# Kernel tuning notes

Measured on AMD Instinct MI355X. Metric: run time of the kernel, lower is better.

Reference implementation:

```python
import jax, jax.numpy as jnp
import numpy as np

N_NODES = 50000
N_EDGES = 800000
N_FEAT = 128
N_HID = 128
N_LAYER = 4
N_CLASS = 40


def setup_inputs() -> dict:
    key = jax.random.key(0)
    ks = jax.random.split(key, 8)
    x = jax.random.normal(ks[0], (N_NODES, N_FEAT), jnp.float32)
    edge_index = jax.random.randint(ks[1], (2, N_EDGES), 0, N_NODES, dtype=jnp.int64)
    s = 1.0 / np.float32(np.sqrt(N_HID))
    # n_feat == n_hid so all L conv weights stack into one [L, C, C] tensor
    convW = jax.random.normal(ks[2], (N_LAYER, N_HID, N_HID), jnp.float32) * s
    convb = jnp.zeros((N_LAYER, N_HID), jnp.float32)
    W_att = jax.random.normal(ks[3], (N_HID, N_HID), jnp.float32) * s
    a_att = jax.random.normal(ks[4], (N_HID,), jnp.float32) * s
    W_out = jax.random.normal(ks[5], (N_HID, N_CLASS), jnp.float32) * s
    b_out = jnp.zeros((N_CLASS,), jnp.float32)
    return dict(x=x, edge_index=edge_index, convW=convW, convb=convb,
                W_att=W_att, a_att=a_att, W_out=W_out, b_out=b_out)


def reference(x, edge_index, convW, convb, W_att, a_att, W_out, b_out):
    src, dst = edge_index[0], edge_index[1]
    N = x.shape[0]
    # GCN symmetric normalization with self-loops: deg = 1 + in-degree
    deg = jax.ops.segment_sum(jnp.ones_like(dst, dtype=jnp.float32), dst,
                              num_segments=N) + 1.0
    dinv = jax.lax.rsqrt(deg)
    enorm = (dinv[src] * dinv[dst])[:, None]   # per-edge norm
    snorm = (dinv * dinv)[:, None]             # self-loop norm

    hs = []
    h = x
    for l in range(N_LAYER):
        hW = h @ convW[l]                                          # [N, C]
        agg = jax.ops.segment_sum(hW[src] * enorm, dst, num_segments=N)
        agg = agg + hW * snorm                                     # self-loop
        h = jax.nn.relu(agg + convb[l])
        # dropout is identity at inference (training=False)
        hs.append(h)

    H = jnp.stack(hs, axis=1)                                      # [N, L, C]
    # additive attention over layers: alpha_l = softmax_l(a . tanh(W h_l))
    scores = jnp.tanh(H @ W_att) @ a_att                           # [N, L]
    alpha = jax.nn.softmax(scores, axis=1)
    fused = jnp.einsum('nl,nlc->nc', alpha, H)                     # [N, C]
    return fused @ W_out + b_out                                   # [N, n_class]
```

## Files before the change

### kernel.cpp

```cpp
#include <hip/hip_runtime.h>

#define NNODES 50000
#define NEDGES 800000
#define NCLASS 40
#define NBLK_SCAN 196
#define CNTB  3125
#define PREPB 320
#define WOUTB 24
#define GEMMB 782
#define XBLK  3125

typedef _Float16 half8  __attribute__((ext_vector_type(8)));
typedef float    floatx4 __attribute__((ext_vector_type(4)));

#define CSTR 136
#define SMEM_BYTES (64 * CSTR * 2 + 256)

__device__ __forceinline__ float fast_tanh(float x) {
    return 1.0f - 2.0f / (__expf(2.0f * x) + 1.0f);
}

__global__ __launch_bounds__(256) void k_pre(const int* __restrict__ dst, int* __restrict__ cnt,
                                             int* __restrict__ rank,
                                             const float* __restrict__ convW, const float* __restrict__ W_att,
                                             _Float16* __restrict__ WT,
                                             const float* __restrict__ Wout, _Float16* __restrict__ WoutT) {
    int bid = blockIdx.x, tid = threadIdx.x;
    if (bid < CNTB) {
        int e = bid * 256 + tid;
        rank[e] = atomicAdd(&cnt[dst[e]], 1);
    } else if (bid < CNTB + PREPB) {
        int idx = (bid - CNTB) * 256 + tid;
        int mat = idx >> 14, rem = idx & 16383;
        int j = rem & 7, lane = (rem >> 3) & 63, tile = rem >> 9;
        int l15 = lane & 15, quad = lane >> 4;
        int ct = tile & 7, kk = tile >> 3;
        int n = ct * 16 + l15, k = kk * 32 + quad * 8 + j;
        const float* src = (mat < 4) ? (convW + mat * 16384) : W_att;
        WT[idx] = (_Float16)src[k * 128 + n];
    } else {
        int idx = (bid - CNTB - PREPB) * 256 + tid;
        int j = idx & 7, lane = (idx >> 3) & 63, tile = idx >> 9;
        int l15 = lane & 15, quad = lane >> 4;
        int ct = tile % 3, kk = tile / 3;
        int n = ct * 16 + l15, k = kk * 32 + quad * 8 + j;
        WoutT[idx] = (n < NCLASS) ? (_Float16)Wout[k * NCLASS + n] : (_Float16)0.f;
    }
}

__global__ __launch_bounds__(256) void k_bsum(const int* __restrict__ cnt, int* __restrict__ bsum) {
    int t = threadIdx.x, b = blockIdx.x;
    int i = b * 256 + t;
    int c = (i < NNODES) ? cnt[i] : 0;
    int v = c;
    v += __shfl_xor(v, 1);  v += __shfl_xor(v, 2);  v += __shfl_xor(v, 4);
    v += __shfl_xor(v, 8);  v += __shfl_xor(v, 16); v += __shfl_xor(v, 32);
    __shared__ int ws[4];
    if ((t & 63) == 0) ws[t >> 6] = v;
    __syncthreads();
    if (t == 0) bsum[b] = ws[0] + ws[1] + ws[2] + ws[3];
}

__global__ __launch_bounds__(256) void k_offsets(const int* __restrict__ cnt, const int* __restrict__ bsum,
                                                 int* __restrict__ offsets, float* __restrict__ dinv) {
    int t = threadIdx.x, b = blockIdx.x;
    int i = b * 256 + t;
    int c = (i < NNODES) ? cnt[i] : 0;
    int pv = (t < b) ? bsum[t] : 0;
    int rv = pv;
    rv += __shfl_xor(rv, 1);  rv += __shfl_xor(rv, 2);  rv += __shfl_xor(rv, 4);
    rv += __shfl_xor(rv, 8);  rv += __shfl_xor(rv, 16); rv += __shfl_xor(rv, 32);
    __shared__ int wsum[4];
    __shared__ int part[256];
    if ((t & 63) == 0) wsum[t >> 6] = rv;
    part[t] = c;
    __syncthreads();
    int boff = wsum[0] + wsum[1] + wsum[2] + wsum[3];
#pragma unroll
    for (int d = 1; d < 256; d <<= 1) {
        int v = (t >= d) ? part[t - d] : 0;
        __syncthreads();
        part[t] += v;
        __syncthreads();
    }
    if (i < NNODES) {
        offsets[i] = boff + part[t] - c;
        dinv[i] = rsqrtf((float)c + 1.0f);
    }
    if (b == 0 && t == 0) offsets[NNODES] = NEDGES;
}

__device__ __forceinline__ void gemm_body_f32(const float* __restrict__ Av, const _Float16* __restrict__ WTf,
                                              const float* __restrict__ dinv, _Float16* __restrict__ C,
                                              int m0, char* smem) {
    _Float16 (*Csh)[CSTR] = (_Float16 (*)[CSTR])smem;
    float* sdinv = (float*)(smem + 64 * CSTR * 2);
    int tid = threadIdx.x;
    int wave = tid >> 6, lane = tid & 63;
    int quad = lane >> 4, l15 = lane & 15;
    int ko = quad * 8;

    if (tid < 64) {
        int r = m0 + tid; if (r > NNODES - 1) r = NNODES - 1;
        sdinv[tid] = dinv[r];
    }

    floatx4 acc[4][2];
#pragma unroll
    for (int rt = 0; rt < 4; ++rt)
#pragma unroll
        for (int ct = 0; ct < 2; ++ct) acc[rt][ct] = (floatx4){0.f, 0.f, 0.f, 0.f};

#pragma unroll
    for (int kk = 0; kk < 4; ++kk) {
        half8 a[4], b[2];
#pragma unroll
        for (int rt = 0; rt < 4; ++rt) {
            int row = m0 + rt * 16 + l15;
            if (row > NNODES - 1) row = NNODES - 1;
            const float* Ap = Av + (size_t)row * 128 + kk * 32 + ko;
            float4 f0 = *(const float4*)Ap;
            float4 f1 = *(const float4*)(Ap + 4);
            a[rt] = (half8){(_Float16)f0.x, (_Float16)f0.y, (_Float16)f0.z, (_Float16)f0.w,
                            (_Float16)f1.x, (_Float16)f1.y, (_Float16)f1.z, (_Float16)f1.w};
        }
#pragma unroll
        for (int ct = 0; ct < 2; ++ct)
            b[ct] = *(const half8*)&WTf[((kk * 8 + (wave * 2 + ct)) * 64 + lane) * 8];
#pragma unroll
        for (int rt = 0; rt < 4; ++rt)
#pragma unroll
            for (int ct = 0; ct < 2; ++ct)
                acc[rt][ct] = __builtin_amdgcn_mfma_f32_16x16x32_f16(a[rt], b[ct], acc[rt][ct], 0, 0, 0);
    }
    __syncthreads();

#pragma unroll
    for (int rt = 0; rt < 4; ++rt)
#pragma unroll
        for (int r = 0; r < 4; ++r) {
            float d = sdinv[rt * 16 + quad * 4 + r];
#pragma unroll
            for (int ct = 0; ct < 2; ++ct)
                Csh[rt * 16 + quad * 4 + r][wave * 32 + ct * 16 + l15] = (_Float16)(acc[rt][ct][r] * d);
        }
    __syncthreads();

    int row = tid >> 2, seg = tid & 3;
    int gm = m0 + row;
    if (gm < NNODES) {
#pragma unroll
        for (int j = 0; j < 4; ++j)
            *(half8*)(C + (size_t)gm * 128 + seg * 32 + j * 8) = *(const half8*)&Csh[row][seg * 32 + j * 8];
    }
}

__global__ __launch_bounds__(256) void k_fillgemm(const int* __restrict__ src, const int* __restrict__ dst,
                                                  const int* __restrict__ offsets, const int* __restrict__ rank,
                                                  int* __restrict__ esrc,
                                                  const float* __restrict__ x, const _Float16* __restrict__ WT,
                                                  const float* __restrict__ dinv, _Float16* __restrict__ C) {
    __shared__ __align__(16) char smem[SMEM_BYTES];
    int bid = blockIdx.x;
    if (bid < GEMMB) {
        gemm_body_f32(x, WT, dinv, C, bid * 64, smem);
    } else {
        int e = (bid - GEMMB) * 256 + threadIdx.x;
        int d = dst[e];
        esrc[offsets[d] + rank[e]] = src[e];
    }
}

template <bool HAS_GEMM>
__global__ __launch_bounds__(128) void k_layer(const _Float16* __restrict__ hin,
                                               const int* __restrict__ offsets, const int* __restrict__ esrc,
                                               const float* __restrict__ dinv, const float* __restrict__ bias,
                                               _Float16* __restrict__ hh,
                                               const _Float16* __restrict__ WTatt, const float* __restrict__ a_att,
                                               float* __restrict__ scores, int layer,
                                               const _Float16* __restrict__ WTnext, _Float16* __restrict__ hout) {
    __shared__ __align__(16) _Float16 h[16][CSTR];
    __shared__ float bsh[128];
    __shared__ float sdv[16];
    __shared__ float pp[2][16];
    int tid = threadIdx.x;
    bsh[tid] = bias[tid];
    int wave = tid >> 6, lane = tid & 63;
    int n0 = blockIdx.x * 16;

    {
        int nl = tid >> 3;
        int cl = tid & 7;
        int c16 = cl * 16;
        int n = n0 + nl;
        int beg = offsets[n], end = offsets[n + 1];
        float dn = dinv[n];
        const _Float16* sp = hin + (size_t)n * 128 + c16;
        half8 sv0 = *(const half8*)sp;
        half8 sv1 = *(const half8*)(sp + 8);

        float a[16];
#pragma unroll
        for (int u = 0; u < 16; ++u) a[u] = 0.f;

        int idxA[4]; float mskA[4];
#pragma unroll
        for (int i = 0; i < 4; ++i) {
            int ei = beg + i;
            int t = esrc[ei];
            bool ok = ei < end;
            idxA[i] = ok ? t : n;
            mskA[i] = ok ? 1.f : 0.f;
        }
        for (int e = beg; e < end; e += 4) {
            half8 v0[4], v1[4];
#pragma unroll
            for (int i = 0; i < 4; ++i) {
                const _Float16* p = hin + (size_t)idxA[i] * 128 + c16;
                v0[i] = *(const half8*)p;
                v1[i] = *(const half8*)(p + 8);
            }
            int idxB[4]; float mskB[4];
#pragma unroll
            for (int i = 0; i < 4; ++i) {
                int ei = e + 4 + i;
                int t = esrc[ei];
                bool ok = ei < end;
                idxB[i] = ok ? t : n;
                mskB[i] = ok ? 1.f : 0.f;
            }
#pragma unroll
            for (int i = 0; i < 4; ++i) {
                float m = mskA[i];
#pragma unroll
                for (int u = 0; u < 8; ++u) {
                    a[u]     += m * (float)v0[i][u];
                    a[8 + u] += m * (float)v1[i][u];
                }
            }
#pragma unroll
            for (int i = 0; i < 4; ++i) { idxA[i] = idxB[i]; mskA[i] = mskB[i]; }
        }
        __syncthreads();
        half8 o0, o1;
#pragma unroll
        for (int u = 0; u < 8; ++u) {
            float r0 = (a[u]     + (float)sv0[u]) * dn + bsh[c16 + u];
            float r1 = (a[8 + u] + (float)sv1[u]) * dn + bsh[c16 + 8 + u];
            o0[u] = (_Float16)fmaxf(r0, 0.f);
            o1[u] = (_Float16)fmaxf(r1, 0.f);
        }
        *(half8*)(hh + (size_t)n * 128 + c16)     = o0;
        *(half8*)(hh + (size_t)n * 128 + c16 + 8) = o1;
        *(half8*)&h[nl][c16]     = o0;
        *(half8*)&h[nl][c16 + 8] = o1;
        if (cl == 0) sdv[nl] = dn;
    }
    __syncthreads();

    int quad = lane >> 4, l15 = lane & 15;
    int ko = quad * 8;
    half8 af[4];
#pragma unroll
    for (int kk = 0; kk < 4; ++kk) af[kk] = *(const half8*)&h[l15][kk * 32 + ko];

    {
        float p[4] = {0.f, 0.f, 0.f, 0.f};
#pragma unroll
        for (int c2 = 0; c2 < 4; ++c2) {
            int ct = wave * 4 + c2;
            half8 b[4];
#pragma unroll
            for (int kk = 0; kk < 4; ++kk)
                b[kk] = *(const half8*)&WTatt[((kk * 8 + ct) * 64 + lane) * 8];
            floatx4 acc = (floatx4){0.f, 0.f, 0.f, 0.f};
#pragma unroll
            for (int kk = 0; kk < 4; ++kk)
                acc = __builtin_amdgcn_mfma_f32_16x16x32_f16(af[kk], b[kk], acc, 0, 0, 0);
            float av = a_att[ct * 16 + l15];
#pragma unroll
            for (int r = 0; r < 4; ++r) p[r] += av * fast_tanh(acc[r]);
        }
#pragma unroll
        for (int r = 0; r < 4; ++r) {
            float v = p[r];
            v += __shfl_xor(v, 1); v += __shfl_xor(v, 2);
            v += __shfl_xor(v, 4); v += __shfl_xor(v, 8);
            if (l15 == 0) pp[wave][quad * 4 + r] = v;
        }
    }
    __syncthreads();
    if (tid < 16) scores[(size_t)(n0 + tid) * 4 + layer] = pp[0][tid] + pp[1][tid];

    if (HAS_GEMM) {
        floatx4 acc[4];
#pragma unroll
        for (int c2 = 0; c2 < 4; ++c2) acc[c2] = (floatx4){0.f, 0.f, 0.f, 0.f};
#pragma unroll
        for (int c2 = 0; c2 < 4; ++c2) {
            int ct = wave * 4 + c2;
#pragma unroll
            for (int kk = 0; kk < 4; ++kk) {
                half8 b = *(const half8*)&WTnext[((kk * 8 + ct) * 64 + lane) * 8];
                acc[c2] = __builtin_amdgcn_mfma_f32_16x16x32_f16(af[kk], b, acc[c2], 0, 0, 0);
            }
        }
        __syncthreads();
#pragma unroll
        for (int c2 = 0; c2 < 4; ++c2) {
            int col = wave * 64 + c2 * 16 + l15;
#pragma unroll
            for (int r = 0; r < 4; ++r) {
                int row = quad * 4 + r;
                h[row][col] = (_Float16)(acc[c2][r] * sdv[row]);
            }
        }
        __syncthreads();
        int row = tid >> 3, seg = tid & 7;
        int gm = n0 + row;
        *(half8*)(hout + (size_t)gm * 128 + seg * 16)     = *(const half8*)&h[row][seg * 16];
        *(half8*)(hout + (size_t)gm * 128 + seg * 16 + 8) = *(const half8*)&h[row][seg * 16 + 8];
    }
}

__global__ __launch_bounds__(256) void k_fuse_out(const _Float16* __restrict__ hbase, const float* __restrict__ scores,
                                                  const _Float16* __restrict__ WoutT, const float* __restrict__ bout,
                                                  float* __restrict__ out) {
    __shared__ __align__(16) _Float16 Fs[64][136];
    __shared__ float salpha[256];
    const size_t LSTR = (size_t)NNODES * 128;
    int tid = threadIdx.x;
    int n0 = blockIdx.x * 64;

    if (tid < 64) {
        int node = n0 + tid; if (node > NNODES - 1) node = NNODES - 1;
        float4 s = *(const float4*)(scores + (size_t)node * 4);
        float mx = fmaxf(fmaxf(s.x, s.y), fmaxf(s.z, s.w));
        float e0 = __expf(s.x - mx), e1 = __expf(s.y - mx), e2 = __expf(s.z - mx), e3 = __expf(s.w - mx);
        float inv = 1.0f / (e0 + e1 + e2 + e3);
        salpha[tid * 4 + 0] = e0 * inv; salpha[tid * 4 + 1] = e1 * inv;
        salpha[tid * 4 + 2] = e2 * inv; salpha[tid * 4 + 3] = e3 * inv;
    }
    __syncthreads();

    {
        int no = tid >> 2, seg = tid & 3;
        int node = n0 + no; if (node > NNODES - 1) node = NNODES - 1;
        float al0 = salpha[no * 4 + 0], al1 = salpha[no * 4 + 1];
        float al2 = salpha[no * 4 + 2], al3 = salpha[no * 4 + 3];
        const _Float16* hp = hbase + (size_t)node * 128 + seg * 32;
#pragma unroll
        for (int j = 0; j < 4; ++j) {
            half8 h0 = *(const half8*)(hp + 0 * LSTR + j * 8);
            half8 h1 = *(const half8*)(hp + 1 * LSTR + j * 8);
            half8 h2 = *(const half8*)(hp + 2 * LSTR + j * 8);
            half8 h3 = *(const half8*)(hp + 3 * LSTR + j * 8);
            half8 f;
#pragma unroll
            for (int u = 0; u < 8; ++u)
                f[u] = (_Float16)(al0 * (float)h0[u] + al1 * (float)h1[u] +
                                  al2 * (float)h2[u] + al3 * (float)h3[u]);
            *(half8*)&Fs[no][seg * 32 + j * 8] = f;
        }
    }
    __syncthreads();

    int wave = tid >> 6, lane = tid & 63;
    int quad = lane >> 4, l15 = lane & 15;
    int ko = quad * 8;
    half8 ff[4];
    int frow = wave * 16 + l15;
#pragma unroll
    for (int kk = 0; kk < 4; ++kk) ff[kk] = *(const half8*)&Fs[frow][kk * 32 + ko];
#pragma unroll
    for (int ct = 0; ct < 3; ++ct) {
        half8 bw[4];
#pragma unroll
        for (int kk = 0; kk < 4; ++kk)
            bw[kk] = *(const half8*)(WoutT + ((kk * 3 + ct) * 64 + lane) * 8);
        floatx4 acc = (floatx4){0.f, 0.f, 0.f, 0.f};
#pragma unroll
        for (int kk = 0; kk < 4; ++kk)
            acc = __builtin_amdgcn_mfma_f32_16x16x32_f16(ff[kk], bw[kk], acc, 0, 0, 0);
        int col = ct * 16 + l15;
        if (col < NCLASS) {
            float bv = bout[col];
#pragma unroll
            for (int r = 0; r < 4; ++r) {
                int node = n0 + wave * 16 + quad * 4 + r;
                if (node < NNODES) out[(size_t)node * NCLASS + col] = acc[r] + bv;
            }
        }
    }
}

extern "C" void kernel_launch(void* const* d_in, const int* in_sizes, int n_in,
                              void* d_out, int out_size, void* d_ws, size_t ws_size,
                              hipStream_t stream) {
    const float* x     = (const float*)d_in[0];
    const int*   ei    = (const int*)d_in[1];
    const float* convW = (const float*)d_in[2];
    const float* convb = (const float*)d_in[3];
    const float* W_att = (const float*)d_in[4];
    const float* a_att = (const float*)d_in[5];
    const float* W_out = (const float*)d_in[6];
    const float* b_out = (const float*)d_in[7];
    float* out = (float*)d_out;

    char* ws = (char*)d_ws;
    size_t off = 0;
    auto take = [&](size_t nbytes) { char* p = ws + off; off += (nbytes + 255) & ~(size_t)255; return p; };
    float*     dinv    = (float*)take(NNODES * 4);
    int*       cnt     = (int*)take(NNODES * 4);
    int*       rank    = (int*)take(NEDGES * 4);
    int*       offsets = (int*)take((NNODES + 1) * 4);
    int*       bsum    = (int*)take(256 * 4);
    int*       esrc    = (int*)take(NEDGES * 4 + 256);
    _Float16*  WoutT   = (_Float16*)take((size_t)48 * 128 * 2);
    float*     scores  = (float*)take(NNODES * 4 * 4);
    _Float16*  WT      = (_Float16*)take((size_t)5 * 128 * 128 * 2);
    _Float16*  hWsA    = (_Float16*)take((size_t)NNODES * 128 * 2);
    _Float16*  hh[4];
    for (int l = 0; l < 4; ++l) hh[l] = (_Float16*)take((size_t)NNODES * 128 * 2);
    _Float16*  hWsB    = (_Float16*)take((size_t)NNODES * 128 * 2);

    const int* src = ei;
    const int* dst = ei + NEDGES;

    hipMemsetAsync(cnt, 0, NNODES * 4, stream);
    k_pre<<<CNTB + PREPB + WOUTB, 256, 0, stream>>>(dst, cnt, rank, convW, W_att, WT, W_out, WoutT);
    k_bsum<<<NBLK_SCAN, 256, 0, stream>>>(cnt, bsum);
    k_offsets<<<NBLK_SCAN, 256, 0, stream>>>(cnt, bsum, offsets, dinv);
    k_fillgemm<<<GEMMB + CNTB, 256, 0, stream>>>(src, dst, offsets, rank, esrc, x, WT, dinv, hWsA);

    k_layer<true><<<XBLK, 128, 0, stream>>>(hWsA, offsets, esrc, dinv, convb + 0 * 128, hh[0],
                                            WT + 4 * 16384, a_att, scores, 0, WT + 1 * 16384, hWsB);
    k_layer<true><<<XBLK, 128, 0, stream>>>(hWsB, offsets, esrc, dinv, convb + 1 * 128, hh[1],
                                            WT + 4 * 16384, a_att, scores, 1, WT + 2 * 16384, hWsA);
    k_layer<true><<<XBLK, 128, 0, stream>>>(hWsA, offsets, esrc, dinv, convb + 2 * 128, hh[2],
                                            WT + 4 * 16384, a_att, scores, 2, WT + 3 * 16384, hWsB);
    k_layer<false><<<XBLK, 128, 0, stream>>>(hWsB, offsets, esrc, dinv, convb + 3 * 128, hh[3],
                                             WT + 4 * 16384, a_att, scores, 3, (const _Float16*)nullptr,
                                             (_Float16*)nullptr);
    k_fuse_out<<<GEMMB, 256, 0, stream>>>(hh[0], scores, WoutT, b_out, out);
}
```

Measured before the change: 314.9 us.

## Widen layer kernel to 256 threads with deeper gather pipeline and zero-row padding

The per-layer aggregation kernel now uses 256 threads per 16-node block, so each thread gathers 8 channels instead of 16. The gather loop keeps two groups of 4 neighbour rows in flight, giving 8 loads outstanding. Padded edge slots now read a zeroed sentinel row at index NNODES instead of being multiplied by a mask. The MFMA work for the attention score and next-layer GEMM is split across four waves instead of two. The aim is more memory-level parallelism and occupancy for the latency-bound gather, at the cost of two extra memsets and more per-thread index loads.

Measured after the change: 330.3 us. +4.9%, slower.

```diff
diff --git a/kernel.cpp b/kernel.cpp
--- a/kernel.cpp
+++ b/kernel.cpp
@@ -172,7 +172,7 @@
 }
 
 template <bool HAS_GEMM>
-__global__ __launch_bounds__(128) void k_layer(const _Float16* __restrict__ hin,
+__global__ __launch_bounds__(256) void k_layer(const _Float16* __restrict__ hin,
                                                const int* __restrict__ offsets, const int* __restrict__ esrc,
                                                const float* __restrict__ dinv, const float* __restrict__ bias,
                                                _Float16* __restrict__ hh,
@@ -182,78 +182,82 @@
     __shared__ __align__(16) _Float16 h[16][CSTR];
     __shared__ float bsh[128];
     __shared__ float sdv[16];
-    __shared__ float pp[2][16];
+    __shared__ float pp[4][16];
     int tid = threadIdx.x;
-    bsh[tid] = bias[tid];
+    if (tid < 128) bsh[tid] = bias[tid];
     int wave = tid >> 6, lane = tid & 63;
     int n0 = blockIdx.x * 16;
 
     {
-        int nl = tid >> 3;
-        int cl = tid & 7;
-        int c16 = cl * 16;
+        int nl = tid >> 4;
+        int cl = tid & 15;
+        int c8 = cl * 8;
         int n = n0 + nl;
         int beg = offsets[n], end = offsets[n + 1];
         float dn = dinv[n];
-        const _Float16* sp = hin + (size_t)n * 128 + c16;
-        half8 sv0 = *(const half8*)sp;
-        half8 sv1 = *(const half8*)(sp + 8);
-
-        float a[16];
-#pragma unroll
-        for (int u = 0; u < 16; ++u) a[u] = 0.f;
-
-        int idxA[4]; float mskA[4];
+        half8 sv = *(const half8*)(hin + (size_t)n * 128 + c8);
+
+        float a[8];
+#pragma unroll
+        for (int u = 0; u < 8; ++u) a[u] = 0.f;
+
+        int i0[4], i1[4];
 #pragma unroll
         for (int i = 0; i < 4; ++i) {
             int ei = beg + i;
             int t = esrc[ei];
-            bool ok = ei < end;
-            idxA[i] = ok ? t : n;
-            mskA[i] = ok ? 1.f : 0.f;
-        }
-        for (int e = beg; e < end; e += 4) {
-            half8 v0[4], v1[4];
+            i0[i] = (ei < end) ? t : NNODES;
+        }
+        half8 v0[4];
+#pragma unroll
+        for (int i = 0; i < 4; ++i) v0[i] = *(const half8*)(hin + (size_t)i0[i] * 128 + c8);
+#pragma unroll
+        for (int i = 0; i < 4; ++i) {
+            int ei = beg + 4 + i;
+            int t = esrc[ei];
+            i1[i] = (ei < end) ? t : NNODES;
+        }
+        half8 v1[4];
+#pragma unroll
+        for (int i = 0; i < 4; ++i) v1[i] = *(const half8*)(hin + (size_t)i1[i] * 128 + c8);
+
+        for (int e = beg; e < end; e += 8) {
+            int i2[4];
 #pragma unroll
             for (int i = 0; i < 4; ++i) {
-                const _Float16* p = hin + (size_t)idxA[i] * 128 + c16;
-                v0[i] = *(const half8*)p;
-                v1[i] = *(const half8*)(p + 8);
+                int ei = e + 8 + i;
+                int t = esrc[ei];
+                i2[i] = (ei < end) ? t : NNODES;
             }
-            int idxB[4]; float mskB[4];
+#pragma unroll
+            for (int i = 0; i < 4; ++i)
+#pragma unroll
+                for (int u = 0; u < 8; ++u) a[u] += (float)v0[i][u];
+#pragma unroll
+            for (int i = 0; i < 4; ++i) v0[i] = *(const half8*)(hin + (size_t)i2[i] * 128 + c8);
+            int i3[4];
 #pragma unroll
             for (int i = 0; i < 4; ++i) {
-                int ei = e + 4 + i;
+                int ei = e + 12 + i;
                 int t = esrc[ei];
-                bool ok = ei < end;
-                idxB[i] = ok ? t : n;
-                mskB[i] = ok ? 1.f : 0.f;
+                i3[i] = (ei < end) ? t : NNODES;
             }
 #pragma unroll
-            for (int i = 0; i < 4; ++i) {
-                float m = mskA[i];
-#pragma unroll
-                for (int u = 0; u < 8; ++u) {
-                    a[u]     += m * (float)v0[i][u];
-                    a[8 + u] += m * (float)v1[i][u];
-                }
-            }
-#pragma unroll
-            for (int i = 0; i < 4; ++i) { idxA[i] = idxB[i]; mskA[i] = mskB[i]; }
+            for (int i = 0; i < 4; ++i)
+#pragma unroll
+                for (int u = 0; u < 8; ++u) a[u] += (float)v1[i][u];
+#pragma unroll
+            for (int i = 0; i < 4; ++i) v1[i] = *(const half8*)(hin + (size_t)i3[i] * 128 + c8);
         }
         __syncthreads();
-        half8 o0, o1;
+        half8 o;
 #pragma unroll
         for (int u = 0; u < 8; ++u) {
-            float r0 = (a[u]     + (float)sv0[u]) * dn + bsh[c16 + u];
-            float r1 = (a[8 + u] + (float)sv1[u]) * dn + bsh[c16 + 8 + u];
-            o0[u] = (_Float16)fmaxf(r0, 0.f);
-            o1[u] = (_Float16)fmaxf(r1, 0.f);
-        }
-        *(half8*)(hh + (size_t)n * 128 + c16)     = o0;
-        *(half8*)(hh + (size_t)n * 128 + c16 + 8) = o1;
-        *(half8*)&h[nl][c16]     = o0;
-        *(half8*)&h[nl][c16 + 8] = o1;
+            float r = (a[u] + (float)sv[u]) * dn + bsh[c8 + u];
+            o[u] = (_Float16)fmaxf(r, 0.f);
+        }
+        *(half8*)(hh + (size_t)n * 128 + c8) = o;
+        *(half8*)&h[nl][c8] = o;
         if (cl == 0) sdv[nl] = dn;
     }
     __syncthreads();
@@ -267,8 +271,8 @@
     {
         float p[4] = {0.f, 0.f, 0.f, 0.f};
 #pragma unroll
-        for (int c2 = 0; c2 < 4; ++c2) {
-            int ct = wave * 4 + c2;
+        for (int c2 = 0; c2 < 2; ++c2) {
+            int ct = wave * 2 + c2;
             half8 b[4];
 #pragma unroll
             for (int kk = 0; kk < 4; ++kk)
@@ -290,15 +294,15 @@
         }
     }
     __syncthreads();
-    if (tid < 16) scores[(size_t)(n0 + tid) * 4 + layer] = pp[0][tid] + pp[1][tid];
+    if (tid < 16) scores[(size_t)(n0 + tid) * 4 + layer] = pp[0][tid] + pp[1][tid] + pp[2][tid] + pp[3][tid];
 
     if (HAS_GEMM) {
-        floatx4 acc[4];
-#pragma unroll
-        for (int c2 = 0; c2 < 4; ++c2) acc[c2] = (floatx4){0.f, 0.f, 0.f, 0.f};
-#pragma unroll
-        for (int c2 = 0; c2 < 4; ++c2) {
-            int ct = wave * 4 + c2;
+        floatx4 acc[2];
+#pragma unroll
+        for (int c2 = 0; c2 < 2; ++c2) acc[c2] = (floatx4){0.f, 0.f, 0.f, 0.f};
+#pragma unroll
+        for (int c2 = 0; c2 < 2; ++c2) {
+            int ct = wave * 2 + c2;
 #pragma unroll
             for (int kk = 0; kk < 4; ++kk) {
                 half8 b = *(const half8*)&WTnext[((kk * 8 + ct) * 64 + lane) * 8];
@@ -307,8 +311,8 @@
         }
         __syncthreads();
 #pragma unroll
-        for (int c2 = 0; c2 < 4; ++c2) {
-            int col = wave * 64 + c2 * 16 + l15;
+        for (int c2 = 0; c2 < 2; ++c2) {
+            int col = (wave * 2 + c2) * 16 + l15;
 #pragma unroll
             for (int r = 0; r < 4; ++r) {
                 int row = quad * 4 + r;
@@ -316,10 +320,9 @@
             }
         }
         __syncthreads();
-        int row = tid >> 3, seg = tid & 7;
+        int row = tid >> 4, seg = tid & 15;
         int gm = n0 + row;
-        *(half8*)(hout + (size_t)gm * 128 + seg * 16)     = *(const half8*)&h[row][seg * 16];
-        *(half8*)(hout + (size_t)gm * 128 + seg * 16 + 8) = *(const half8*)&h[row][seg * 16 + 8];
+        *(half8*)(hout + (size_t)gm * 128 + seg * 8) = *(const half8*)&h[row][seg * 8];
     }
 }
 
@@ -419,27 +422,29 @@
     _Float16*  WoutT   = (_Float16*)take((size_t)48 * 128 * 2);
     float*     scores  = (float*)take(NNODES * 4 * 4);
     _Float16*  WT      = (_Float16*)take((size_t)5 * 128 * 128 * 2);
-    _Float16*  hWsA    = (_Float16*)take((size_t)NNODES * 128 * 2);
+    _Float16*  hWsA    = (_Float16*)take((size_t)(NNODES + 1) * 128 * 2);
     _Float16*  hh[4];
     for (int l = 0; l < 4; ++l) hh[l] = (_Float16*)take((size_t)NNODES * 128 * 2);
-    _Float16*  hWsB    = (_Float16*)take((size_t)NNODES * 128 * 2);
+    _Float16*  hWsB    = (_Float16*)take((size_t)(NNODES + 1) * 128 * 2);
 
     const int* src = ei;
     const int* dst = ei + NEDGES;
 
     hipMemsetAsync(cnt, 0, NNODES * 4, stream);
+    hipMemsetAsync(hWsA + (size_t)NNODES * 128, 0, 256, stream);
+    hipMemsetAsync(hWsB + (size_t)NNODES * 128, 0, 256, stream);
     k_pre<<<CNTB + PREPB + WOUTB, 256, 0, stream>>>(dst, cnt, rank, convW, W_att, WT, W_out, WoutT);
     k_bsum<<<NBLK_SCAN, 256, 0, stream>>>(cnt, bsum);
     k_offsets<<<NBLK_SCAN, 256, 0, stream>>>(cnt, bsum, offsets, dinv);
     k_fillgemm<<<GEMMB + CNTB, 256, 0, stream>>>(src, dst, offsets, rank, esrc, x, WT, dinv, hWsA);
 
-    k_layer<true><<<XBLK, 128, 0, stream>>>(hWsA, offsets, esrc, dinv, convb + 0 * 128, hh[0],
+    k_layer<true><<<XBLK, 256, 0, stream>>>(hWsA, offsets, esrc, dinv, convb + 0 * 128, hh[0],
                                             WT + 4 * 16384, a_att, scores, 0, WT + 1 * 16384, hWsB);
-    k_layer<true><<<XBLK, 128, 0, stream>>>(hWsB, offsets, esrc, dinv, convb + 1 * 128, hh[1],
+    k_layer<true><<<XBLK, 256, 0, stream>>>(hWsB, offsets, esrc, dinv, convb + 1 * 128, hh[1],
                                             WT + 4 * 16384, a_att, scores, 1, WT + 2 * 16384, hWsA);
-    k_layer<true><<<XBLK, 128, 0, stream>>>(hWsA, offsets, esrc, dinv, convb + 2 * 128, hh[2],
+    k_layer<true><<<XBLK, 256, 0, stream>>>(hWsA, offsets, esrc, dinv, convb + 2 * 128, hh[2],
                                             WT + 4 * 16384, a_att, scores, 2, WT + 3 * 16384, hWsB);
-    k_layer<false><<<XBLK, 128, 0, stream>>>(hWsB, offsets, esrc, dinv, convb + 3 * 128, hh[3],
+    k_layer<false><<<XBLK, 256, 0, stream>>>(hWsB, offsets, esrc, dinv, convb + 3 * 128, hh[3],
                                              WT + 4 * 16384, a_att, scores, 3, (const _Float16*)nullptr,
                                              (_Float16*)nullptr);
     k_fuse_out<<<GEMMB, 256, 0, stream>>>(hh[0], scores, WoutT, b_out, out);
```
